# Kernel tuning notes

Hardware: AMD Instinct MI355X
Metric: run time of the kernel (lower is better)

The kernel has to match this reference:

```python
import jax, jax.numpy as jnp
import numpy as np

N_NODES = 50000
N_EDGES = 800000
HEADS = 4
OUT_CH = 32
IN_CH = 128
EPS_LN = 1e-5
NEG_SLOPE = 0.2


def setup_inputs() -> dict:
    key = jax.random.key(0)
    ks = jax.random.split(key, 6)
    x = jax.random.normal(ks[0], (N_NODES, IN_CH), dtype=jnp.float32)
    edge_index = jax.random.randint(ks[1], (2, N_EDGES), 0, N_NODES, dtype=jnp.int64)
    # PyG GATConv lin weight (glorot-ish scale), attention vectors, bias, LN params
    W = jax.random.normal(ks[2], (IN_CH, HEADS * OUT_CH), dtype=jnp.float32) / np.sqrt(IN_CH)
    att_src = jax.random.normal(ks[3], (HEADS, OUT_CH), dtype=jnp.float32) / np.sqrt(OUT_CH)
    att_dst = jax.random.normal(ks[4], (HEADS, OUT_CH), dtype=jnp.float32) / np.sqrt(OUT_CH)
    bias = jnp.zeros((HEADS * OUT_CH,), dtype=jnp.float32)
    gamma = jnp.ones((HEADS * OUT_CH,), dtype=jnp.float32)
    beta = jnp.zeros((HEADS * OUT_CH,), dtype=jnp.float32)
    return {"x": x, "edge_index": edge_index, "W": W, "att_src": att_src,
            "att_dst": att_dst, "bias": bias, "gamma": gamma, "beta": beta}


def reference(x, edge_index, W, att_src, att_dst, bias, gamma, beta):
    N = x.shape[0]
    # --- GATConv (concat=True, add_self_loops=True, dropout disabled) ---
    h = (x @ W).reshape(N, HEADS, OUT_CH)                 # [N, H, C]
    a_src = jnp.einsum("nhc,hc->nh", h, att_src)          # [N, H]
    a_dst = jnp.einsum("nhc,hc->nh", h, att_dst)          # [N, H]
    loop = jnp.arange(N, dtype=edge_index.dtype)
    src = jnp.concatenate([edge_index[0], loop])          # [E+N]
    dst = jnp.concatenate([edge_index[1], loop])          # [E+N]
    e = jax.nn.leaky_relu(a_src[src] + a_dst[dst], NEG_SLOPE)  # [E+N, H]
    # segment softmax over incoming edges of each dst node (stable)
    m = jax.ops.segment_max(e, dst, num_segments=N)       # [N, H]
    e = jnp.exp(e - m[dst])
    denom = jax.ops.segment_sum(e, dst, num_segments=N)   # [N, H]
    alpha = e / (denom[dst] + 1e-16)                      # [E+N, H]
    msg = alpha[:, :, None] * h[src]                      # [E+N, H, C]
    out = jax.ops.segment_sum(msg, dst, num_segments=N)   # [N, H, C]
    out = out.reshape(N, HEADS * OUT_CH) + bias
    # --- ELU, (dropout=identity), residual (in==out_dim), LayerNorm ---
    out = jax.nn.elu(out) + x
    mu = out.mean(-1, keepdims=True)
    var = out.var(-1, keepdims=True)
    out = (out - mu) * jax.lax.rsqrt(var + EPS_LN) * gamma + beta
    return out
```

## Files before the change

### kernel.cpp

```cpp
#include <hip/hip_runtime.h>
#include <hip/hip_bf16.h>

constexpr int N_NODES = 50000;
constexpr int N_EDGES = 800000;
constexpr int EN      = N_EDGES + N_NODES;
constexpr int HEADS   = 4;
constexpr int OUT_CH  = 32;
constexpr int HC      = HEADS * OUT_CH;
constexpr float NEG_SLOPE = 0.2f;
constexpr float EPS_LN    = 1e-5f;

__global__ __launch_bounds__(128)
void gemm_att(const float* __restrict__ x, const float* __restrict__ W,
              const float* __restrict__ att_s, const float* __restrict__ att_d,
              float* __restrict__ h, float* __restrict__ asrc, float* __restrict__ adst) {
    __shared__ float Wl[HC * HC];
    __shared__ float xs[8][HC];
    const int t = threadIdx.x;
    for (int i = t; i < HC * HC; i += 128) Wl[i] = W[i];
    const float as = att_s[t];
    const float ad = att_d[t];
    const int lane = t & 63;
    const int head = t >> 5;

    for (int row0 = blockIdx.x * 8; row0 < N_NODES; row0 += gridDim.x * 8) {
        __syncthreads();
        #pragma unroll
        for (int r = 0; r < 8; ++r)
            xs[r][t] = x[(size_t)(row0 + r) * HC + t];
        __syncthreads();

        float acc[8];
        #pragma unroll
        for (int r = 0; r < 8; ++r) acc[r] = 0.f;

        for (int k = 0; k < HC; k += 4) {
            const float w0 = Wl[(k + 0) * HC + t];
            const float w1 = Wl[(k + 1) * HC + t];
            const float w2 = Wl[(k + 2) * HC + t];
            const float w3 = Wl[(k + 3) * HC + t];
            #pragma unroll
            for (int r = 0; r < 8; ++r) {
                const float4 xv = *(const float4*)&xs[r][k];
                acc[r] += w0 * xv.x + w1 * xv.y + w2 * xv.z + w3 * xv.w;
            }
        }

        #pragma unroll
        for (int r = 0; r < 8; ++r) {
            h[(size_t)(row0 + r) * HC + t] = acc[r];
            float vs = acc[r] * as;
            float vd = acc[r] * ad;
            #pragma unroll
            for (int s = 16; s >= 1; s >>= 1) {
                vs += __shfl_xor(vs, s, 64);
                vd += __shfl_xor(vd, s, 64);
            }
            if ((lane & 31) == 0) {
                asrc[(row0 + r) * HEADS + head] = vs;
                adst[(row0 + r) * HEADS + head] = vd;
            }
        }
    }
}

__global__ __launch_bounds__(256)
void deg_hist(const int* __restrict__ ei, unsigned* __restrict__ deg) {
    const int e = blockIdx.x * 256 + threadIdx.x;
    if (e >= EN) return;
    const int dst = (e < N_EDGES) ? ei[N_EDGES + e] : (e - N_EDGES);
    atomicAdd(&deg[dst], 1u);
}

__global__ __launch_bounds__(1024)
void scan_rows(const unsigned* __restrict__ deg, unsigned* __restrict__ rs) {
    __shared__ unsigned wsum[16];
    const int tid = threadIdx.x, lane = tid & 63, w = tid >> 6;
    unsigned carry = 0;
    for (int base = 0; base < N_NODES; base += 1024) {
        const int i = base + tid;
        const unsigned v = (i < N_NODES) ? deg[i] : 0u;
        unsigned incl = v;
        #pragma unroll
        for (int off = 1; off < 64; off <<= 1) {
            const unsigned nb = __shfl_up(incl, off, 64);
            if (lane >= off) incl += nb;
        }
        if (lane == 63) wsum[w] = incl;
        __syncthreads();
        unsigned woff = 0, total = 0;
        #pragma unroll
        for (int j = 0; j < 16; ++j) {
            if (j < w) woff += wsum[j];
            total += wsum[j];
        }
        if (i < N_NODES) rs[i] = carry + woff + incl - v;
        carry += total;
        __syncthreads();
    }
    if (tid == 0) rs[N_NODES] = carry;
}

__global__ __launch_bounds__(256)
void scatter_edges(const int* __restrict__ ei, const unsigned* __restrict__ rs,
                   unsigned* __restrict__ cursor, int* __restrict__ esrc) {
    const int e = blockIdx.x * 256 + threadIdx.x;
    if (e >= EN) return;
    const int src = (e < N_EDGES) ? ei[e] : (e - N_EDGES);
    const int dst = (e < N_EDGES) ? ei[N_EDGES + e] : (e - N_EDGES);
    const unsigned pos = rs[dst] + atomicAdd(&cursor[dst], 1u);
    esrc[pos] = src;
}

__global__ __launch_bounds__(128)
void gat_aggregate(const int* __restrict__ esrc, const unsigned* __restrict__ rs,
                   const float* __restrict__ asrc, const float* __restrict__ adst,
                   const float* __restrict__ h, const float* __restrict__ x,
                   const float* __restrict__ bias, const float* __restrict__ gamma,
                   const float* __restrict__ beta, float* __restrict__ out) {
    const int n = blockIdx.x;
    const int t = threadIdx.x;
    const int hh = t >> 5;
    const int start = (int)rs[n], end = (int)rs[n + 1];
    const float adn = adst[n * HEADS + hh];

    float m = -INFINITY, s = 0.f, acc = 0.f;
    int pos = start;
    for (; pos + 1 < end; pos += 2) {
        const int s0 = esrc[pos], s1 = esrc[pos + 1];
        float v0 = asrc[s0 * HEADS + hh] + adn;
        float v1 = asrc[s1 * HEADS + hh] + adn;
        v0 = (v0 > 0.f) ? v0 : NEG_SLOPE * v0;
        v1 = (v1 > 0.f) ? v1 : NEG_SLOPE * v1;
        const float h0 = h[(size_t)s0 * HC + t];
        const float h1 = h[(size_t)s1 * HC + t];
        const float nm = fmaxf(m, fmaxf(v0, v1));
        const float c  = expf(m - nm);
        const float w0 = expf(v0 - nm);
        const float w1 = expf(v1 - nm);
        acc = acc * c + w0 * h0 + w1 * h1;
        s   = s   * c + w0 + w1;
        m = nm;
    }
    if (pos < end) {
        const int s0 = esrc[pos];
        float v0 = asrc[s0 * HEADS + hh] + adn;
        v0 = (v0 > 0.f) ? v0 : NEG_SLOPE * v0;
        const float h0 = h[(size_t)s0 * HC + t];
        const float nm = fmaxf(m, v0);
        const float c  = expf(m - nm);
        const float w0 = expf(v0 - nm);
        acc = acc * c + w0 * h0;
        s   = s   * c + w0;
    }

    float o = acc / (s + 1e-16f) + bias[t];
    o = (o > 0.f) ? o : expm1f(o);
    o += x[(size_t)n * HC + t];

    __shared__ float red[4];
    float ss = o, sq = o * o;
    #pragma unroll
    for (int off = 32; off >= 1; off >>= 1) {
        ss += __shfl_xor(ss, off, 64);
        sq += __shfl_xor(sq, off, 64);
    }
    const int w = t >> 6;
    if ((t & 63) == 0) { red[w * 2] = ss; red[w * 2 + 1] = sq; }
    __syncthreads();
    const float S = red[0] + red[2], Q = red[1] + red[3];
    const float mu   = S * (1.f / HC);
    const float var  = Q * (1.f / HC) - mu * mu;
    const float rstd = rsqrtf(var + EPS_LN);
    out[(size_t)n * HC + t] = (o - mu) * rstd * gamma[t] + beta[t];
}

extern "C" void kernel_launch(void* const* d_in, const int* in_sizes, int n_in,
                              void* d_out, int out_size, void* d_ws, size_t ws_size,
                              hipStream_t stream) {
    const float* x     = (const float*)d_in[0];
    const int*   ei    = (const int*)  d_in[1];
    const float* W     = (const float*)d_in[2];
    const float* att_s = (const float*)d_in[3];
    const float* att_d = (const float*)d_in[4];
    const float* bias  = (const float*)d_in[5];
    const float* gamma = (const float*)d_in[6];
    const float* beta  = (const float*)d_in[7];
    float* out = (float*)d_out;

    char* ws = (char*)d_ws;
    float*    h      = (float*)   (ws);
    float*    asrc   = (float*)   (ws + 25600000);
    float*    adst   = (float*)   (ws + 26400000);
    unsigned* deg    = (unsigned*)(ws + 27200000);
    unsigned* cursor = (unsigned*)(ws + 27400000);
    unsigned* rs     = (unsigned*)(ws + 27600000);
    int*      esrc   = (int*)     (ws + 27800192);

    hipMemsetAsync(deg,    0, (size_t)N_NODES * 4, stream);
    hipMemsetAsync(cursor, 0, (size_t)N_NODES * 4, stream);

    gemm_att<<<512, 128, 0, stream>>>(x, W, att_s, att_d, h, asrc, adst);

    const int e_grid = (EN + 255) / 256;
    deg_hist     <<<e_grid, 256, 0, stream>>>(ei, deg);
    scan_rows    <<<1, 1024, 0, stream>>>(deg, rs);
    scatter_edges<<<e_grid, 256, 0, stream>>>(ei, rs, cursor, esrc);

    gat_aggregate<<<N_NODES, 128, 0, stream>>>(esrc, rs, asrc, adst, h, x,
                                               bias, gamma, beta, out);
}
```

Measured before the change: 412.4 us.

## Register-resident W GEMM, multi-block scan, one-wave-per-node aggregation

Measured after the change: 978.1 us. 2.37x slower.

```diff
diff --git a/kernel.cpp b/kernel.cpp
--- a/kernel.cpp
+++ b/kernel.cpp
@@ -10,55 +10,54 @@
 constexpr float NEG_SLOPE = 0.2f;
 constexpr float EPS_LN    = 1e-5f;
 
-__global__ __launch_bounds__(128)
+constexpr int SCAN_BLK = 1024;
+constexpr int SCAN_NB  = (N_NODES + SCAN_BLK - 1) / SCAN_BLK;
+
+__global__ __launch_bounds__(256, 4)
 void gemm_att(const float* __restrict__ x, const float* __restrict__ W,
               const float* __restrict__ att_s, const float* __restrict__ att_d,
-              float* __restrict__ h, float* __restrict__ asrc, float* __restrict__ adst) {
-    __shared__ float Wl[HC * HC];
-    __shared__ float xs[8][HC];
-    const int t = threadIdx.x;
-    for (int i = t; i < HC * HC; i += 128) Wl[i] = W[i];
-    const float as = att_s[t];
-    const float ad = att_d[t];
+              float* __restrict__ h, float* __restrict__ asrc, float* __restrict__ adst)
+{
+    const int t    = threadIdx.x;
+    const int c    = t >> 1;
+    const int kg   = t & 1;
     const int lane = t & 63;
-    const int head = t >> 5;
-
-    for (int row0 = blockIdx.x * 8; row0 < N_NODES; row0 += gridDim.x * 8) {
-        __syncthreads();
+    const int wv   = t >> 6;
+
+    float Wr[64];
+    #pragma unroll
+    for (int j = 0; j < 64; ++j)
+        Wr[j] = W[(kg * 64 + j) * HC + c];
+
+    const float as = att_s[c];
+    const float ad = att_d[c];
+
+    for (int row0 = blockIdx.x * 4; row0 < N_NODES; row0 += gridDim.x * 4) {
+        float acc[4] = {0.f, 0.f, 0.f, 0.f};
         #pragma unroll
-        for (int r = 0; r < 8; ++r)
-            xs[r][t] = x[(size_t)(row0 + r) * HC + t];
-        __syncthreads();
-
-        float acc[8];
-        #pragma unroll
-        for (int r = 0; r < 8; ++r) acc[r] = 0.f;
-
-        for (int k = 0; k < HC; k += 4) {
-            const float w0 = Wl[(k + 0) * HC + t];
-            const float w1 = Wl[(k + 1) * HC + t];
-            const float w2 = Wl[(k + 2) * HC + t];
-            const float w3 = Wl[(k + 3) * HC + t];
+        for (int r = 0; r < 4; ++r) {
+            const float4* xr = (const float4*)(x + (size_t)(row0 + r) * HC + kg * 64);
             #pragma unroll
-            for (int r = 0; r < 8; ++r) {
-                const float4 xv = *(const float4*)&xs[r][k];
-                acc[r] += w0 * xv.x + w1 * xv.y + w2 * xv.z + w3 * xv.w;
+            for (int j = 0; j < 16; ++j) {
+                const float4 xv = xr[j];
+                acc[r] += Wr[4*j+0] * xv.x + Wr[4*j+1] * xv.y
+                        + Wr[4*j+2] * xv.z + Wr[4*j+3] * xv.w;
             }
         }
-
         #pragma unroll
-        for (int r = 0; r < 8; ++r) {
-            h[(size_t)(row0 + r) * HC + t] = acc[r];
-            float vs = acc[r] * as;
-            float vd = acc[r] * ad;
+        for (int r = 0; r < 4; ++r) {
+            const float accf = acc[r] + __shfl_xor(acc[r], 1, 64);
+            if (kg == 0) h[(size_t)(row0 + r) * HC + c] = accf;
+            float vs = accf * as;
+            float vd = accf * ad;
             #pragma unroll
-            for (int s = 16; s >= 1; s >>= 1) {
-                vs += __shfl_xor(vs, s, 64);
-                vd += __shfl_xor(vd, s, 64);
+            for (int mb = 2; mb <= 32; mb <<= 1) {
+                vs += __shfl_xor(vs, mb, 64);
+                vd += __shfl_xor(vd, mb, 64);
             }
-            if ((lane & 31) == 0) {
-                asrc[(row0 + r) * HEADS + head] = vs;
-                adst[(row0 + r) * HEADS + head] = vd;
+            if (lane == 0) {
+                asrc[(row0 + r) * HEADS + wv] = vs;
+                adst[(row0 + r) * HEADS + wv] = vd;
             }
         }
     }
@@ -72,33 +71,53 @@
     atomicAdd(&deg[dst], 1u);
 }
 
-__global__ __launch_bounds__(1024)
-void scan_rows(const unsigned* __restrict__ deg, unsigned* __restrict__ rs) {
+__global__ __launch_bounds__(SCAN_BLK)
+void scan_part(const unsigned* __restrict__ deg, unsigned* __restrict__ rs,
+               unsigned* __restrict__ bsum)
+{
     __shared__ unsigned wsum[16];
     const int tid = threadIdx.x, lane = tid & 63, w = tid >> 6;
-    unsigned carry = 0;
-    for (int base = 0; base < N_NODES; base += 1024) {
-        const int i = base + tid;
-        const unsigned v = (i < N_NODES) ? deg[i] : 0u;
-        unsigned incl = v;
-        #pragma unroll
-        for (int off = 1; off < 64; off <<= 1) {
-            const unsigned nb = __shfl_up(incl, off, 64);
-            if (lane >= off) incl += nb;
-        }
-        if (lane == 63) wsum[w] = incl;
-        __syncthreads();
-        unsigned woff = 0, total = 0;
-        #pragma unroll
-        for (int j = 0; j < 16; ++j) {
-            if (j < w) woff += wsum[j];
-            total += wsum[j];
-        }
-        if (i < N_NODES) rs[i] = carry + woff + incl - v;
-        carry += total;
-        __syncthreads();
-    }
-    if (tid == 0) rs[N_NODES] = carry;
+    const int i = blockIdx.x * SCAN_BLK + tid;
+    const unsigned v = (i < N_NODES) ? deg[i] : 0u;
+    unsigned incl = v;
+    #pragma unroll
+    for (int off = 1; off < 64; off <<= 1) {
+        const unsigned nb = __shfl_up(incl, off, 64);
+        if (lane >= off) incl += nb;
+    }
+    if (lane == 63) wsum[w] = incl;
+    __syncthreads();
+    unsigned woff = 0, total = 0;
+    #pragma unroll
+    for (int j = 0; j < 16; ++j) {
+        const unsigned tv = wsum[j];
+        if (j < w) woff += tv;
+        total += tv;
+    }
+    if (i < N_NODES) rs[i] = woff + incl - v;
+    if (tid == 0) bsum[blockIdx.x] = total;
+}
+
+__global__ __launch_bounds__(64)
+void scan_tops(unsigned* __restrict__ bsum)
+{
+    const int lane = threadIdx.x;
+    const unsigned v = (lane < SCAN_NB) ? bsum[lane] : 0u;
+    unsigned incl = v;
+    #pragma unroll
+    for (int off = 1; off < 64; off <<= 1) {
+        const unsigned nb = __shfl_up(incl, off, 64);
+        if (lane >= off) incl += nb;
+    }
+    if (lane < SCAN_NB) bsum[lane] = incl - v;
+}
+
+__global__ __launch_bounds__(SCAN_BLK)
+void scan_add(const unsigned* __restrict__ bsum, unsigned* __restrict__ rs)
+{
+    const int i = blockIdx.x * SCAN_BLK + threadIdx.x;
+    if (i < N_NODES) rs[i] += bsum[blockIdx.x];
+    if (i == 0) rs[N_NODES] = (unsigned)EN;
 }
 
 __global__ __launch_bounds__(256)
@@ -112,19 +131,21 @@
     esrc[pos] = src;
 }
 
-__global__ __launch_bounds__(128)
+__global__ __launch_bounds__(256, 4)
 void gat_aggregate(const int* __restrict__ esrc, const unsigned* __restrict__ rs,
                    const float* __restrict__ asrc, const float* __restrict__ adst,
                    const float* __restrict__ h, const float* __restrict__ x,
                    const float* __restrict__ bias, const float* __restrict__ gamma,
-                   const float* __restrict__ beta, float* __restrict__ out) {
-    const int n = blockIdx.x;
-    const int t = threadIdx.x;
-    const int hh = t >> 5;
+                   const float* __restrict__ beta, float* __restrict__ out)
+{
+    const int wv   = threadIdx.x >> 6;
+    const int lane = threadIdx.x & 63;
+    const int n    = blockIdx.x * 4 + wv;
+    const int hh   = lane >> 4;
     const int start = (int)rs[n], end = (int)rs[n + 1];
     const float adn = adst[n * HEADS + hh];
 
-    float m = -INFINITY, s = 0.f, acc = 0.f;
+    float m = -INFINITY, s = 0.f, ax = 0.f, ay = 0.f;
     int pos = start;
     for (; pos + 1 < end; pos += 2) {
         const int s0 = esrc[pos], s1 = esrc[pos + 1];
@@ -132,47 +153,54 @@
         float v1 = asrc[s1 * HEADS + hh] + adn;
         v0 = (v0 > 0.f) ? v0 : NEG_SLOPE * v0;
         v1 = (v1 > 0.f) ? v1 : NEG_SLOPE * v1;
-        const float h0 = h[(size_t)s0 * HC + t];
-        const float h1 = h[(size_t)s1 * HC + t];
+        const float2 h0 = ((const float2*)(h + (size_t)s0 * HC))[lane];
+        const float2 h1 = ((const float2*)(h + (size_t)s1 * HC))[lane];
         const float nm = fmaxf(m, fmaxf(v0, v1));
-        const float c  = expf(m - nm);
+        const float cs = expf(m - nm);
         const float w0 = expf(v0 - nm);
         const float w1 = expf(v1 - nm);
-        acc = acc * c + w0 * h0 + w1 * h1;
-        s   = s   * c + w0 + w1;
+        ax = ax * cs + w0 * h0.x + w1 * h1.x;
+        ay = ay * cs + w0 * h0.y + w1 * h1.y;
+        s  = s  * cs + w0 + w1;
         m = nm;
     }
     if (pos < end) {
         const int s0 = esrc[pos];
         float v0 = asrc[s0 * HEADS + hh] + adn;
         v0 = (v0 > 0.f) ? v0 : NEG_SLOPE * v0;
-        const float h0 = h[(size_t)s0 * HC + t];
+        const float2 h0 = ((const float2*)(h + (size_t)s0 * HC))[lane];
         const float nm = fmaxf(m, v0);
-        const float c  = expf(m - nm);
+        const float cs = expf(m - nm);
         const float w0 = expf(v0 - nm);
-        acc = acc * c + w0 * h0;
-        s   = s   * c + w0;
-    }
-
-    float o = acc / (s + 1e-16f) + bias[t];
-    o = (o > 0.f) ? o : expm1f(o);
-    o += x[(size_t)n * HC + t];
-
-    __shared__ float red[4];
-    float ss = o, sq = o * o;
+        ax = ax * cs + w0 * h0.x;
+        ay = ay * cs + w0 * h0.y;
+        s  = s  * cs + w0;
+    }
+
+    const float inv = 1.f / (s + 1e-16f);
+    const float2 bv = ((const float2*)bias)[lane];
+    const float2 xv = ((const float2*)(x + (size_t)n * HC))[lane];
+    float ox = ax * inv + bv.x;
+    float oy = ay * inv + bv.y;
+    ox = (ox > 0.f) ? ox : expm1f(ox);
+    oy = (oy > 0.f) ? oy : expm1f(oy);
+    ox += xv.x; oy += xv.y;
+
+    float ss = ox + oy, sq = ox * ox + oy * oy;
     #pragma unroll
     for (int off = 32; off >= 1; off >>= 1) {
         ss += __shfl_xor(ss, off, 64);
         sq += __shfl_xor(sq, off, 64);
     }
-    const int w = t >> 6;
-    if ((t & 63) == 0) { red[w * 2] = ss; red[w * 2 + 1] = sq; }
-    __syncthreads();
-    const float S = red[0] + red[2], Q = red[1] + red[3];
-    const float mu   = S * (1.f / HC);
-    const float var  = Q * (1.f / HC) - mu * mu;
+    const float mu   = ss * (1.f / HC);
+    const float var  = sq * (1.f / HC) - mu * mu;
     const float rstd = rsqrtf(var + EPS_LN);
-    out[(size_t)n * HC + t] = (o - mu) * rstd * gamma[t] + beta[t];
+    const float2 gv = ((const float2*)gamma)[lane];
+    const float2 bt = ((const float2*)beta)[lane];
+    float2 ov;
+    ov.x = (ox - mu) * rstd * gv.x + bt.x;
+    ov.y = (oy - mu) * rstd * gv.y + bt.y;
+    ((float2*)(out + (size_t)n * HC))[lane] = ov;
 }
 
 extern "C" void kernel_launch(void* const* d_in, const int* in_sizes, int n_in,
@@ -195,18 +223,21 @@
     unsigned* deg    = (unsigned*)(ws + 27200000);
     unsigned* cursor = (unsigned*)(ws + 27400000);
     unsigned* rs     = (unsigned*)(ws + 27600000);
-    int*      esrc   = (int*)     (ws + 27800192);
+    unsigned* bsum   = (unsigned*)(ws + 27800192);
+    int*      esrc   = (int*)     (ws + 27800448);
 
     hipMemsetAsync(deg,    0, (size_t)N_NODES * 4, stream);
     hipMemsetAsync(cursor, 0, (size_t)N_NODES * 4, stream);
 
-    gemm_att<<<512, 128, 0, stream>>>(x, W, att_s, att_d, h, asrc, adst);
+    gemm_att<<<1024, 256, 0, stream>>>(x, W, att_s, att_d, h, asrc, adst);
 
     const int e_grid = (EN + 255) / 256;
     deg_hist     <<<e_grid, 256, 0, stream>>>(ei, deg);
-    scan_rows    <<<1, 1024, 0, stream>>>(deg, rs);
+    scan_part    <<<SCAN_NB, SCAN_BLK, 0, stream>>>(deg, rs, bsum);
+    scan_tops    <<<1, 64, 0, stream>>>(bsum);
+    scan_add     <<<SCAN_NB, SCAN_BLK, 0, stream>>>(bsum, rs);
     scatter_edges<<<e_grid, 256, 0, stream>>>(ei, rs, cursor, esrc);
 
-    gat_aggregate<<<N_NODES, 128, 0, stream>>>(esrc, rs, asrc, adst, h, x,
-                                               bias, gamma, beta, out);
-}
+    gat_aggregate<<<N_NODES / 4, 256, 0, stream>>>(esrc, rs, asrc, adst, h, x,
+                                                   bias, gamma, beta, out);
+}
```
